# Optimization experiments

Measured on AMD Instinct MI355X. Metric: run time of the kernel, lower is better.

The kernel has to match this reference:

```python
import jax, jax.numpy as jnp
import numpy as np
import math

B, L = 4, 4096
D_MODEL = 1024
D_INNER = 1024          # expand=1
D_STATE = 1             # required by rearrange 'b d 1 l' in ssm()
D_CONV = 2
DT_RANK = 64            # ceil(1024/16)
EPS = 1e-5


def setup_inputs() -> dict:
    key = jax.random.key(0)
    ks = jax.random.split(key, 8)
    dt_min, dt_max, dt_floor = 1e-3, 1e-1, 1e-4
    # dt_proj bias init: inverse-softplus of log-uniform dt (faithful to dt_init)
    dt = jnp.exp(jax.random.uniform(ks[5], (D_INNER,)) * (math.log(dt_max) - math.log(dt_min)) + math.log(dt_min))
    dt = jnp.clip(dt, dt_floor, None)
    inv_dt = dt + jnp.log(-jnp.expm1(-dt))
    std = DT_RANK ** -0.5
    return {
        "x": jax.random.normal(ks[0], (B, L, D_MODEL), dtype=jnp.float32),
        "w_in": jax.random.normal(ks[1], (2 * D_INNER, D_MODEL), dtype=jnp.float32) * 0.02,
        "conv_w": jax.random.normal(ks[2], (D_INNER, 1, D_CONV), dtype=jnp.float32) * 0.5,
        "conv_b": jnp.zeros((D_INNER,), dtype=jnp.float32),
        "x_proj_weight": jax.random.normal(ks[3], (DT_RANK + 2 * D_STATE, D_INNER), dtype=jnp.float32) * 0.02,
        "dt_projs_weight": jax.random.uniform(ks[4], (D_INNER, DT_RANK), minval=-std, maxval=std, dtype=jnp.float32),
        "dt_projs_bias": inv_dt,
        "A_logs": jnp.tile(jnp.log(jnp.arange(1, D_STATE + 1, dtype=jnp.float32))[None, :], (D_INNER, 1)),
        "Ds": jnp.ones((D_INNER,), dtype=jnp.float32),
        "ln_w": jnp.ones((D_INNER,), dtype=jnp.float32),
        "ln_b": jnp.zeros((D_INNER,), dtype=jnp.float32),
        "w_out": jax.random.normal(ks[6], (D_MODEL, D_INNER), dtype=jnp.float32) * 0.02,
    }


def _selective_scan(u, delta, A, Bs):
    # u, delta: (B, D, L); A: (D, N); Bs: (B, N, L) -> hidden states h: (B, D, N, L)
    dA = jnp.exp(jnp.einsum('bdl,dn->bdnl', delta, A))            # (B,D,N,L)
    dBu = jnp.einsum('bdl,bnl,bdl->bdnl', delta, Bs, u)           # delta * B * u
    dA_t = jnp.moveaxis(dA, -1, 0)                                # (L,B,D,N)
    dBu_t = jnp.moveaxis(dBu, -1, 0)

    def step(h, inp):
        a_t, bu_t = inp
        h = a_t * h + bu_t
        return h, h

    h0 = jnp.zeros(dA.shape[:-1], dtype=u.dtype)
    _, hs = jax.lax.scan(step, h0, (dA_t, dBu_t))                 # (L,B,D,N)
    return jnp.moveaxis(hs, 0, -1)                                # (B,D,N,L)


def reference(x, w_in, conv_w, conv_b, x_proj_weight, dt_projs_weight,
              dt_projs_bias, A_logs, Ds, ln_w, ln_b, w_out):
    Bsz, Lsz, _ = x.shape
    # in_proj (bias=False), chunk into x and gate z
    xz = x @ w_in.T                                               # (B,L,2*D)
    xc, z = xz[..., :D_INNER], xz[..., D_INNER:]
    xc = jnp.transpose(xc, (0, 2, 1))                             # (B,D,L)
    # depthwise causal conv1d, padding=d_conv-1, truncated to L
    xc = jax.lax.conv_general_dilated(
        xc, conv_w, window_strides=(1,), padding=[(D_CONV - 1, D_CONV - 1)],
        feature_group_count=D_INNER,
        dimension_numbers=('NCH', 'OIH', 'NCH'))[..., :Lsz]
    xc = xc + conv_b[None, :, None]
    xc = jax.nn.silu(xc)
    # ssm()
    x_dbl = jnp.einsum('rd,bdl->brl', x_proj_weight, xc)          # (B,R+2N,L)
    dts = x_dbl[:, :DT_RANK]
    Bs = x_dbl[:, DT_RANK:DT_RANK + D_STATE]                      # (B,N,L)
    Cs = x_dbl[:, DT_RANK + D_STATE:]                             # (B,N,L)
    dts = jnp.einsum('dr,brl->bdl', dt_projs_weight, dts)         # (B,D,L)
    A = -jnp.exp(A_logs)                                          # (D,N)
    delta = jax.nn.softplus(dts + dt_projs_bias[None, :, None])   # delta_softplus=True
    h = _selective_scan(xc, delta, A, Bs)                         # (B,D,N,L)
    h = h.reshape(Bsz, D_INNER * D_STATE, Lsz)                    # 'b d 1 l -> b (d 1) l' (N==1)
    y = h * Cs + xc * Ds[:, None]                                 # (B,D,L)
    # out_norm (LayerNorm over d_inner), gate, out_proj
    y = jnp.transpose(y, (0, 2, 1))                               # (B,L,D)
    mu = jnp.mean(y, axis=-1, keepdims=True)
    var = jnp.mean(jnp.square(y - mu), axis=-1, keepdims=True)
    y = (y - mu) * jax.lax.rsqrt(var + EPS) * ln_w + ln_b
    y = y * jax.nn.silu(z)
    return y @ w_out.T                                            # (B,L,d_model)
```

## Files before the change

kernel.cpp:

```cpp
#include <hip/hip_runtime.h>
#include <hip/hip_bf16.h>
#include <cstdint>
#include <cstddef>

typedef short short8 __attribute__((ext_vector_type(8)));
typedef short short4v __attribute__((ext_vector_type(4)));
typedef float floatx4 __attribute__((ext_vector_type(4)));

constexpr int Bz = 4;
constexpr int Lz = 4096;
constexpr int Dm = 1024;
constexpr int Di = 1024;
constexpr int Mrows = Bz * Lz;
constexpr int CH  = 32;
constexpr int NCH = Lz / CH;
constexpr int XPJ_KS = 4;

__device__ __forceinline__ void load16(const void* g, void* l) {
  __builtin_amdgcn_global_load_lds((__attribute__((address_space(1))) void*)g,
                                   (__attribute__((address_space(3))) void*)l,
                                   16, 0, 0);
}

__device__ __forceinline__ float bf2f(const __hip_bfloat16 v) { return __bfloat162float(v); }
__device__ __forceinline__ short f2bfs(float v) {
  __hip_bfloat16 h = __float2bfloat16(v);
  return *(short*)&h;
}

__global__ __launch_bounds__(256) void cvt_all(
    const float* __restrict__ x, const float* __restrict__ w_in,
    const float* __restrict__ w_out, const float* __restrict__ xpw,
    const float* __restrict__ dtw,
    __hip_bfloat16* __restrict__ xbf, __hip_bfloat16* __restrict__ w_in_bf,
    __hip_bfloat16* __restrict__ w_out_bf, __hip_bfloat16* __restrict__ xpw_bf,
    __hip_bfloat16* __restrict__ dtw_bf)
{
  const int i = blockIdx.x * 256 + threadIdx.x;
  const float* src; __hip_bfloat16* dst; int j;
  if (i < 4194304)      { src = x;     dst = xbf;      j = i; }
  else if (i < 4718592) { src = w_in;  dst = w_in_bf;  j = i - 4194304; }
  else if (i < 4980736) { src = w_out; dst = w_out_bf; j = i - 4718592; }
  else if (i < 4997632) { src = xpw;   dst = xpw_bf;   j = i - 4980736; }
  else if (i < 5014016) { src = dtw;   dst = dtw_bf;   j = i - 4997632; }
  else return;
  const float4 v = ((const float4*)src)[j];
  short4v s;
  s[0] = f2bfs(v.x); s[1] = f2bfs(v.y); s[2] = f2bfs(v.z); s[3] = f2bfs(v.w);
  ((short4v*)dst)[j] = s;
}

template <int EPI>
__global__ __launch_bounds__(256) void gemm128(
    const __hip_bfloat16* __restrict__ A,
    const __hip_bfloat16* __restrict__ W,
    int K, int N,
    __hip_bfloat16* __restrict__ outb0,
    __hip_bfloat16* __restrict__ outb1,
    float* __restrict__ outf,
    const float* __restrict__ biasf)
{
  constexpr int BK = 32;
  constexpr int GY = 16;
  __shared__ short sA[128 * BK];
  __shared__ short sB[128 * BK];
  const int tid  = threadIdx.x;
  const int wid  = tid >> 6;
  const int lane = tid & 63;

  const int gx  = gridDim.x;
  const int id  = blockIdx.y * gx + blockIdx.x;
  const int seg = gx * GY;
  const int bx  = (id % seg) / GY;
  const int by  = (id / seg) * GY + (id % GY);

  const int m0 = by * 128;
  const int n0 = bx * 128;
  const int wm = (wid & 1) * 64;
  const int wn = (wid >> 1) * 64;

  floatx4 acc[4][4];
#pragma unroll
  for (int i = 0; i < 4; i++)
#pragma unroll
    for (int j = 0; j < 4; j++) acc[i][j] = (floatx4){0.f, 0.f, 0.f, 0.f};

  const short* Ag = (const short*)A + (size_t)(m0 + (tid >> 2)) * K + (tid & 3) * 8;
  const short* Bg = (const short*)W + (size_t)(n0 + (tid >> 2)) * K + (tid & 3) * 8;
  short* sAd = &sA[tid * 8];
  short* sBd = &sB[tid * 8];
  const size_t rstep = (size_t)64 * K;
  const int fr = lane & 15, fq = lane >> 4;

  for (int kb = 0; kb < K; kb += BK) {
    load16(Ag, sAd);
    load16(Ag + rstep, sAd + 2048);
    load16(Bg, sBd);
    load16(Bg + rstep, sBd + 2048);
    Ag += BK; Bg += BK;
    __syncthreads();

    short8 av[4], bv[4];
#pragma unroll
    for (int mt = 0; mt < 4; mt++) av[mt] = *(const short8*)&sA[(wm + mt * 16 + fr) * BK + fq * 8];
#pragma unroll
    for (int nt = 0; nt < 4; nt++) bv[nt] = *(const short8*)&sB[(wn + nt * 16 + fr) * BK + fq * 8];
#pragma unroll
    for (int mt = 0; mt < 4; mt++)
#pragma unroll
      for (int nt = 0; nt < 4; nt++)
        acc[mt][nt] = __builtin_amdgcn_mfma_f32_16x16x32_bf16(av[mt], bv[nt], acc[mt][nt], 0, 0, 0);
    __syncthreads();
  }

#pragma unroll
  for (int mt = 0; mt < 4; mt++) {
#pragma unroll
    for (int nt = 0; nt < 4; nt++) {
#pragma unroll
      for (int r = 0; r < 4; r++) {
        const int gm = m0 + wm + mt * 16 + fq * 4 + r;
        const int gn = n0 + wn + nt * 16 + fr;
        float v = acc[mt][nt][r];
        if constexpr (EPI == 0) {
          if (gn < 1024) outb0[(size_t)gm * 1024 + gn] = __float2bfloat16(v);
          else           outb1[(size_t)gm * 1024 + (gn - 1024)] = __float2bfloat16(v);
        } else if constexpr (EPI == 1) {
          v += biasf[gn];
          v = (v > 15.f) ? v : __logf(1.f + __expf(v));
          outb0[(size_t)gm * N + gn] = __float2bfloat16(v);
        } else {
          outf[(size_t)gm * N + gn] = v;
        }
      }
    }
  }
}

__device__ __forceinline__ void wait_lgkm0() {
  asm volatile("s_waitcnt lgkmcnt(0)");
  __builtin_amdgcn_sched_barrier(0);
}

template <int EPI>
__device__ __forceinline__ void cluster_mfma(int MQ, floatx4 (&acc)[8][4],
                                             const short8 (&av)[8][2],
                                             const short8 (&bv)[4][2])
{
  __builtin_amdgcn_s_setprio(1);
#pragma unroll
  for (int j = 0; j < 2; j++)
#pragma unroll
    for (int nf = 0; nf < 4; nf++)
#pragma unroll
      for (int ks = 0; ks < 2; ks++)
        acc[2 * MQ + j][nf] = __builtin_amdgcn_mfma_f32_16x16x32_bf16(
            av[2 * MQ + j][ks], bv[nf][ks], acc[2 * MQ + j][nf], 0, 0, 0);
  __builtin_amdgcn_s_setprio(0);
}

template <int EPI>
__global__ __launch_bounds__(512, 2) void gemm256(
    const __hip_bfloat16* __restrict__ A,
    const __hip_bfloat16* __restrict__ W,
    int K, int N,
    __hip_bfloat16* __restrict__ outb0,
    __hip_bfloat16* __restrict__ outb1,
    float* __restrict__ outf,
    const float* __restrict__ cw, const float* __restrict__ cb,
    __hip_bfloat16* __restrict__ xef, __hip_bfloat16* __restrict__ xel)
{
  __shared__ alignas(16) char lds[131072];
  const int tid  = threadIdx.x;
  const int wid  = tid >> 6;
  const int lane = tid & 63;
  const int wm = wid >> 2;
  const int wn = wid & 3;
  const int fr = lane & 15, fq = lane >> 4;

  const int gx   = gridDim.x;
  const int nwg  = gx * gridDim.y;
  const int orig = blockIdx.y * gx + blockIdx.x;
  const int swz  = (orig & 7) * (nwg >> 3) + (orig >> 3);
  const int bx   = swz % gx;
  const int by   = swz / gx;
  const int m0 = by * 256;
  const int n0 = bx * 256;
  const size_t K2 = (size_t)K * 2;

  int rowo[2], colo[2];
#pragma unroll
  for (int i = 0; i < 2; i++) {
    const int p = i * 8192 + tid * 16;
    const int s = p >> 10;
    const int r = (p >> 6) & 15;
    rowo[i] = (s >> 1) * 16 + r;
    colo[i] = (s & 1) * 64 + ((p & 63) ^ (((r >> 3) & 1) << 5));
  }
  const char* Ab = (const char*)A + (size_t)m0 * K2;
  const char* Bb = (const char*)W + (size_t)n0 * K2;
  char* lbase = (char*)lds;

#define STAGE_A(c, h, kt) do {                                                          \
    load16(Ab + (size_t)((h) * 128 + rowo[0]) * K2 + (size_t)(kt) * 128 + colo[0],      \
           lbase + (c) * 32768 + (h) * 16384 + tid * 16);                               \
    load16(Ab + (size_t)((h) * 128 + rowo[1]) * K2 + (size_t)(kt) * 128 + colo[1],      \
           lbase + (c) * 32768 + (h) * 16384 + 8192 + tid * 16);                        \
  } while (0)
#define STAGE_B(c, h, kt) do {                                                          \
    load16(Bb + (size_t)((h) * 128 + rowo[0]) * K2 + (size_t)(kt) * 128 + colo[0],      \
           lbase + 65536 + (c) * 32768 + (h) * 16384 + tid * 16);                       \
    load16(Bb + (size_t)((h) * 128 + rowo[1]) * K2 + (size_t)(kt) * 128 + colo[1],      \
           lbase + 65536 + (c) * 32768 + (h) * 16384 + 8192 + tid * 16);                \
  } while (0)

  const int foff = (fr * 64 + fq * 16) ^ (((fr >> 3) & 1) << 5);

  floatx4 acc[8][4];
#pragma unroll
  for (int i = 0; i < 8; i++)
#pragma unroll
    for (int j = 0; j < 4; j++) acc[i][j] = (floatx4){0.f, 0.f, 0.f, 0.f};

  STAGE_A(0, 0, 0); STAGE_A(0, 1, 0); STAGE_B(0, 0, 0); STAGE_B(0, 1, 0);
  STAGE_B(1, 0, 1); STAGE_B(1, 1, 1); STAGE_A(1, 0, 1);
  asm volatile("s_waitcnt vmcnt(6)");
  __builtin_amdgcn_sched_barrier(0);
  __builtin_amdgcn_s_barrier();

  const int NT = K >> 6;
  short8 av[8][2], bv[4][2];
#pragma unroll 2
  for (int t = 0; t < NT; ++t) {
    const int cur = t & 1, nxt = cur ^ 1;
    const char* la = lbase + cur * 32768 + wm * 16384 + foff;
    const char* lb = lbase + 65536 + cur * 32768 + (wn >> 1) * 16384 + (wn & 1) * 8192 + foff;

#pragma unroll
    for (int nf = 0; nf < 4; nf++)
#pragma unroll
      for (int ks = 0; ks < 2; ks++)
        bv[nf][ks] = *(const short8*)(lb + (nf * 2 + ks) * 1024);
#pragma unroll
    for (int mf = 0; mf < 2; mf++)
#pragma unroll
      for (int ks = 0; ks < 2; ks++)
        av[mf][ks] = *(const short8*)(la + (mf * 2 + ks) * 1024);
    if (t + 1 < NT) STAGE_A(nxt, 1, t + 1);
    wait_lgkm0();
    cluster_mfma<EPI>(0, acc, av, bv);
    __builtin_amdgcn_s_barrier();

#pragma unroll
    for (int mf = 2; mf < 4; mf++)
#pragma unroll
      for (int ks = 0; ks < 2; ks++)
        av[mf][ks] = *(const short8*)(la + (mf * 2 + ks) * 1024);
    if (t + 2 < NT) STAGE_B(cur, 0, t + 2);
    wait_lgkm0();
    cluster_mfma<EPI>(1, acc, av, bv);
    __builtin_amdgcn_s_barrier();

#pragma unroll
    for (int mf = 4; mf < 8; mf++)
#pragma unroll
      for (int ks = 0; ks < 2; ks++)
        av[mf][ks] = *(const short8*)(la + (mf * 2 + ks) * 1024);
    if (t + 2 < NT) STAGE_B(cur, 1, t + 2);
    wait_lgkm0();
    cluster_mfma<EPI>(2, acc, av, bv);
    __builtin_amdgcn_s_barrier();

    if (t + 2 < NT) STAGE_A(cur, 0, t + 2);
    cluster_mfma<EPI>(3, acc, av, bv);
    if (t < NT - 2) {
      asm volatile("s_waitcnt vmcnt(6)");
      __builtin_amdgcn_sched_barrier(0);
      __builtin_amdgcn_s_barrier();
    } else if (t == NT - 2) {
      asm volatile("s_waitcnt vmcnt(0)");
      __builtin_amdgcn_sched_barrier(0);
      __builtin_amdgcn_s_barrier();
    }
  }
#undef STAGE_A
#undef STAGE_B

  if constexpr (EPI == 0) {
    if (n0 < 1024) {
      short* lt = (short*)lds;
#pragma unroll
      for (int mf = 0; mf < 8; mf++)
#pragma unroll
        for (int nf = 0; nf < 4; nf++)
#pragma unroll
          for (int r = 0; r < 4; r++)
            lt[(wm * 128 + mf * 16 + fq * 4 + r) * 256 + wn * 64 + nf * 16 + fr] =
                f2bfs(acc[mf][nf][r]);
      __syncthreads();

      const int lrow0 = wid * 2 + (lane >> 5);
      const int c8 = (lane & 31) * 8;
      const int d0 = n0 + c8;
      const float4* cw4 = (const float4*)(cw + 2 * d0);
      const float4 wA = cw4[0], wB = cw4[1], wC = cw4[2], wD = cw4[3];
      const float w0a[8] = {wA.x, wA.z, wB.x, wB.z, wC.x, wC.z, wD.x, wD.z};
      const float w1a[8] = {wA.y, wA.w, wB.y, wB.w, wC.y, wC.w, wD.y, wD.w};
      const float4* cb4 = (const float4*)(cb + d0);
      const float4 b0 = cb4[0], b1 = cb4[1];
      const float ba[8] = {b0.x, b0.y, b0.z, b0.w, b1.x, b1.y, b1.z, b1.w};
      const int tix = m0 >> 8;

      for (int it = 0; it < 16; ++it) {
        const int rl = lrow0 + it * 16;
        const short8 curv = *(const short8*)&lt[rl * 256 + c8];
        if (rl == 0)   *(short8*)((short*)xef + tix * 1024 + d0) = curv;
        if (rl == 255) *(short8*)((short*)xel + tix * 1024 + d0) = curv;
        if (rl == 0) continue;
        const short8 prvv = *(const short8*)&lt[(rl - 1) * 256 + c8];
        short8 outv;
#pragma unroll
        for (int k = 0; k < 8; k++) {
          const float pc = __uint_as_float(((uint32_t)(uint16_t)prvv[k]) << 16);
          const float cc = __uint_as_float(((uint32_t)(uint16_t)curv[k]) << 16);
          const float v = pc * w0a[k] + cc * w1a[k] + ba[k];
          outv[k] = f2bfs(v / (1.f + __expf(-v)));
        }
        *(short8*)((short*)outb0 + (size_t)(m0 + rl) * 1024 + d0) = outv;
      }
    } else {
#pragma unroll
      for (int mf = 0; mf < 8; mf++)
#pragma unroll
        for (int nf = 0; nf < 4; nf++)
#pragma unroll
          for (int r = 0; r < 4; r++) {
            const int gm = m0 + wm * 128 + mf * 16 + fq * 4 + r;
            const int gn = n0 + wn * 64 + nf * 16 + fr;
            outb1[(size_t)gm * 1024 + (gn - 1024)] = __float2bfloat16(acc[mf][nf][r]);
          }
    }
  } else {
#pragma unroll
    for (int mf = 0; mf < 8; mf++)
#pragma unroll
      for (int nf = 0; nf < 4; nf++)
#pragma unroll
        for (int r = 0; r < 4; r++) {
          const int gm = m0 + wm * 128 + mf * 16 + fq * 4 + r;
          const int gn = n0 + wn * 64 + nf * 16 + fr;
          outf[(size_t)gm * N + gn] = acc[mf][nf][r];
        }
  }
}

__global__ __launch_bounds__(256) void conv_fix(
    const __hip_bfloat16* __restrict__ xef, const __hip_bfloat16* __restrict__ xel,
    const float* __restrict__ cw, const float* __restrict__ cb,
    __hip_bfloat16* __restrict__ u)
{
  const int i8 = (blockIdx.x * 256 + threadIdx.x) * 8;
  const int T  = i8 >> 10;
  const int d0 = i8 & 1023;
  const short8 cur = *(const short8*)((const short*)xef + T * 1024 + d0);
  short8 prv;
  if (T & 15) prv = *(const short8*)((const short*)xel + (T - 1) * 1024 + d0);
  else        prv = (short8){0, 0, 0, 0, 0, 0, 0, 0};
  const float4* cw4 = (const float4*)(cw + 2 * d0);
  const float4 wA = cw4[0], wB = cw4[1], wC = cw4[2], wD = cw4[3];
  const float w0a[8] = {wA.x, wA.z, wB.x, wB.z, wC.x, wC.z, wD.x, wD.z};
  const float w1a[8] = {wA.y, wA.w, wB.y, wB.w, wC.y, wC.w, wD.y, wD.w};
  const float4* cb4 = (const float4*)(cb + d0);
  const float4 b0 = cb4[0], b1 = cb4[1];
  const float ba[8] = {b0.x, b0.y, b0.z, b0.w, b1.x, b1.y, b1.z, b1.w};
  short8 outv;
#pragma unroll
  for (int k = 0; k < 8; k++) {
    const float pc = __uint_as_float(((uint32_t)(uint16_t)prv[k]) << 16);
    const float cc = __uint_as_float(((uint32_t)(uint16_t)cur[k]) << 16);
    const float v = pc * w0a[k] + cc * w1a[k] + ba[k];
    outv[k] = f2bfs(v / (1.f + __expf(-v)));
  }
  *(short8*)((short*)u + (size_t)T * 256 * 1024 + d0) = outv;
}

__global__ __launch_bounds__(256) void gemm_xproj(
    const __hip_bfloat16* __restrict__ A,
    const __hip_bfloat16* __restrict__ W,
    float* __restrict__ part)
{
  constexpr int K = 1024, BK = 32, KC = K / XPJ_KS;
  __shared__ short sA[128 * BK];
  __shared__ short sB[80 * BK];
  const int tid = threadIdx.x;
  const int wid = tid >> 6, lane = tid & 63;
  const int kc = blockIdx.x;
  const int m0 = blockIdx.y * 128;

  floatx4 acc[2][5];
#pragma unroll
  for (int i = 0; i < 2; i++)
#pragma unroll
    for (int j = 0; j < 5; j++) acc[i][j] = (floatx4){0.f, 0.f, 0.f, 0.f};

  const short* Ag = (const short*)A + (size_t)(m0 + (tid >> 2)) * K + kc * KC + (tid & 3) * 8;
  const int brow2 = 64 + (tid >> 2);
  const int brow2c = brow2 > 65 ? 65 : brow2;
  const short* Bg  = (const short*)W + (size_t)(tid >> 2) * K + kc * KC + (tid & 3) * 8;
  const short* Bg2 = (const short*)W + (size_t)brow2c * K + kc * KC + (tid & 3) * 8;
  const size_t rstep = (size_t)64 * K;
  const int fr = lane & 15, fq = lane >> 4;

  for (int kb = 0; kb < KC; kb += BK) {
    load16(Ag, &sA[tid * 8]);
    load16(Ag + rstep, &sA[2048 + tid * 8]);
    load16(Bg, &sB[tid * 8]);
    if (tid < 64) load16(Bg2, &sB[2048 + tid * 8]);
    Ag += BK; Bg += BK; Bg2 += BK;
    __syncthreads();

    short8 av[2], bv[5];
#pragma unroll
    for (int mt = 0; mt < 2; mt++) av[mt] = *(const short8*)&sA[(wid * 32 + mt * 16 + fr) * BK + fq * 8];
#pragma unroll
    for (int nt = 0; nt < 5; nt++) bv[nt] = *(const short8*)&sB[(nt * 16 + fr) * BK + fq * 8];
#pragma unroll
    for (int mt = 0; mt < 2; mt++)
#pragma unroll
      for (int nt = 0; nt < 5; nt++)
        acc[mt][nt] = __builtin_amdgcn_mfma_f32_16x16x32_bf16(av[mt], bv[nt], acc[mt][nt], 0, 0, 0);
    __syncthreads();
  }

  float* pp = part + (size_t)kc * Mrows * 66;
#pragma unroll
  for (int mt = 0; mt < 2; mt++) {
#pragma unroll
    for (int nt = 0; nt < 5; nt++) {
#pragma unroll
      for (int r = 0; r < 4; r++) {
        const int gm = m0 + wid * 32 + mt * 16 + fq * 4 + r;
        const int gn = nt * 16 + fr;
        if (gn < 66) pp[(size_t)gm * 66 + gn] = acc[mt][nt][r];
      }
    }
  }
}

__global__ __launch_bounds__(256) void xproj_reduce(
    const float* __restrict__ part,
    __hip_bfloat16* __restrict__ dts,
    float* __restrict__ Bs, float* __restrict__ Cs)
{
  const int i = blockIdx.x * 256 + threadIdx.x;
  if (i >= Mrows * 66) return;
  const int gm = i / 66, gn = i - gm * 66;
  float s = part[i] + part[i + (size_t)Mrows * 66]
          + part[i + (size_t)2 * Mrows * 66] + part[i + (size_t)3 * Mrows * 66];
  if (gn < 64)       dts[(size_t)gm * 64 + gn] = __float2bfloat16(s);
  else if (gn == 64) Bs[gm] = s;
  else               Cs[gm] = s;
}

__global__ __launch_bounds__(256) void scan_p1(
    const __hip_bfloat16* __restrict__ delta, const __hip_bfloat16* __restrict__ u,
    const float* __restrict__ Bsv, const float* __restrict__ A_logs,
    float* __restrict__ carryP, float* __restrict__ carryS)
{
  const int dp = blockIdx.x * 256 + threadIdx.x;
  const int d  = dp * 2;
  const int c = blockIdx.y, b = blockIdx.z;
  const float2 Al = *(const float2*)(A_logs + d);
  const float Ac0 = -__expf(Al.x), Ac1 = -__expf(Al.y);
  const size_t base = ((size_t)(b * Lz + c * CH)) * Di + d;
  const float* Bp = Bsv + (size_t)b * Lz + c * CH;
  float P0 = 1.f, h0 = 0.f, P1 = 1.f, h1 = 0.f;
#pragma unroll 8
  for (int j = 0; j < CH; j++) {
    const uint32_t dv = *(const uint32_t*)((const uint16_t*)delta + base + (size_t)j * Di);
    const uint32_t uv = *(const uint32_t*)((const uint16_t*)u + base + (size_t)j * Di);
    const float dl0 = __uint_as_float(dv << 16);
    const float dl1 = __uint_as_float(dv & 0xffff0000u);
    const float uu0 = __uint_as_float(uv << 16);
    const float uu1 = __uint_as_float(uv & 0xffff0000u);
    const float bj  = Bp[j];
    const float a0 = __expf(dl0 * Ac0), a1 = __expf(dl1 * Ac1);
    h0 = a0 * h0 + dl0 * bj * uu0;
    h1 = a1 * h1 + dl1 * bj * uu1;
    P0 *= a0; P1 *= a1;
  }
  const size_t ci = ((size_t)(b * NCH + c)) * Di + d;
  *(float2*)(carryP + ci) = make_float2(P0, P1);
  *(float2*)(carryS + ci) = make_float2(h0, h1);
}

__global__ __launch_bounds__(64) void scan_p2(
    const float* __restrict__ carryP, const float* __restrict__ carryS,
    float* __restrict__ hin)
{
  const int t = blockIdx.x * 64 + threadIdx.x;
  const int b = t >> 10, d = t & (Di - 1);
  float h = 0.f;
  for (int c = 0; c < NCH; c++) {
    const size_t ci = ((size_t)(b * NCH + c)) * Di + d;
    hin[ci] = h;
    h = carryP[ci] * h + carryS[ci];
  }
}

__global__ __launch_bounds__(256) void scan_p3(
    const __hip_bfloat16* __restrict__ delta, __hip_bfloat16* __restrict__ uy,
    const float* __restrict__ Bsv, const float* __restrict__ Csv,
    const float* __restrict__ A_logs, const float* __restrict__ Ds,
    const float* __restrict__ hin)
{
  const int dp = blockIdx.x * 256 + threadIdx.x;
  const int d  = dp * 2;
  const int c = blockIdx.y, b = blockIdx.z;
  const float2 Al = *(const float2*)(A_logs + d);
  const float Ac0 = -__expf(Al.x), Ac1 = -__expf(Al.y);
  const float2 Dd = *(const float2*)(Ds + d);
  const size_t base = ((size_t)(b * Lz + c * CH)) * Di + d;
  const float* Bp = Bsv + (size_t)b * Lz + c * CH;
  const float* Cp = Csv + (size_t)b * Lz + c * CH;
  const size_t ci = ((size_t)(b * NCH + c)) * Di + d;
  const float2 hh = *(const float2*)(hin + ci);
  float h0 = hh.x, h1 = hh.y;
#pragma unroll 8
  for (int j = 0; j < CH; j++) {
    const size_t ix = base + (size_t)j * Di;
    const uint32_t dv = *(const uint32_t*)((const uint16_t*)delta + ix);
    const uint32_t uv = *(const uint32_t*)((const uint16_t*)uy + ix);
    const float dl0 = __uint_as_float(dv << 16);
    const float dl1 = __uint_as_float(dv & 0xffff0000u);
    const float uu0 = __uint_as_float(uv << 16);
    const float uu1 = __uint_as_float(uv & 0xffff0000u);
    const float bj = Bp[j], cj = Cp[j];
    const float a0 = __expf(dl0 * Ac0), a1 = __expf(dl1 * Ac1);
    h0 = a0 * h0 + dl0 * bj * uu0;
    h1 = a1 * h1 + dl1 * bj * uu1;
    const float y0 = h0 * cj + uu0 * Dd.x;
    const float y1 = h1 * cj + uu1 * Dd.y;
    const uint32_t o = (uint32_t)(uint16_t)f2bfs(y0) | ((uint32_t)(uint16_t)f2bfs(y1) << 16);
    *(uint32_t*)((uint16_t*)uy + ix) = o;
  }
}

__global__ __launch_bounds__(256) void ln_gate(
    const __hip_bfloat16* __restrict__ y, const __hip_bfloat16* __restrict__ z,
    const float* __restrict__ lnw, const float* __restrict__ lnb,
    __hip_bfloat16* __restrict__ yg)
{
  const int row = blockIdx.x;
  const int tid = threadIdx.x;
  const int wid = tid >> 6, lane = tid & 63;
  const short4v yv = *(const short4v*)((const short*)y + (size_t)row * Di + tid * 4);
  const short4v zv4 = *(const short4v*)((const short*)z + (size_t)row * Di + tid * 4);
  float v[4];
#pragma unroll
  for (int i = 0; i < 4; i++)
    v[i] = __uint_as_float(((uint32_t)(uint16_t)yv[i]) << 16);
  float s1 = v[0] + v[1] + v[2] + v[3];
  float s2 = v[0] * v[0] + v[1] * v[1] + v[2] * v[2] + v[3] * v[3];
#pragma unroll
  for (int o = 32; o > 0; o >>= 1) {
    s1 += __shfl_down(s1, o, 64);
    s2 += __shfl_down(s2, o, 64);
  }
  __shared__ float r1[4], r2[4];
  if (lane == 0) { r1[wid] = s1; r2[wid] = s2; }
  __syncthreads();
  const float t1 = r1[0] + r1[1] + r1[2] + r1[3];
  const float t2 = r2[0] + r2[1] + r2[2] + r2[3];
  const float mu = t1 * (1.f / Di);
  const float var = t2 * (1.f / Di) - mu * mu;
  const float rstd = rsqrtf(var + 1e-5f);

  const float4 wv = ((const float4*)lnw)[tid];
  const float4 bv = ((const float4*)lnb)[tid];
  const float wa[4] = {wv.x, wv.y, wv.z, wv.w};
  const float ba[4] = {bv.x, bv.y, bv.z, bv.w};
  short4v og;
#pragma unroll
  for (int i = 0; i < 4; i++) {
    const float zz = __uint_as_float(((uint32_t)(uint16_t)zv4[i]) << 16);
    const float g = zz / (1.f + __expf(-zz));
    og[i] = f2bfs(((v[i] - mu) * rstd * wa[i] + ba[i]) * g);
  }
  *(short4v*)((short*)yg + (size_t)row * Di + tid * 4) = og;
}

__global__ __launch_bounds__(256) void fill_diag(float* __restrict__ out, int n, float val)
{
  const int i = blockIdx.x * 256 + threadIdx.x;
  if (i < n) out[i] = val;
}

extern "C" void kernel_launch(void* const* d_in, const int* in_sizes, int n_in,
                              void* d_out, int out_size, void* d_ws, size_t ws_size,
                              hipStream_t stream)
{
  const float* x      = (const float*)d_in[0];
  const float* w_in   = (const float*)d_in[1];
  const float* conv_w = (const float*)d_in[2];
  const float* conv_b = (const float*)d_in[3];
  const float* xpw    = (const float*)d_in[4];
  const float* dtw    = (const float*)d_in[5];
  const float* dtb    = (const float*)d_in[6];
  const float* A_logs = (const float*)d_in[7];
  const float* Ds     = (const float*)d_in[8];
  const float* lnw    = (const float*)d_in[9];
  const float* lnb    = (const float*)d_in[10];
  const float* w_out  = (const float*)d_in[11];
  float* outF = (float*)d_out;

  const size_t BF16BIG  = (size_t)Mrows * Di * sizeof(__hip_bfloat16);
  const size_t NEED_RUN = 69603328;

  if (ws_size < NEED_RUN) {
    fill_diag<<<(out_size + 255) / 256, 256, 0, stream>>>(
        outF, out_size, (float)(ws_size >> 10));
    return;
  }

  uint8_t* ws = (uint8_t*)d_ws;
  size_t off = 0;
  auto alloc = [&](size_t bytes) { void* p = ws + off; off += (bytes + 255) & ~(size_t)255; return p; };

  __hip_bfloat16* slotA    = (__hip_bfloat16*)alloc(BF16BIG);
  __hip_bfloat16* slotC    = (__hip_bfloat16*)alloc(BF16BIG);
  __hip_bfloat16* w_out_bf = (__hip_bfloat16*)alloc((size_t)Dm * Di * 2);
  __hip_bfloat16* xpw_bf   = (__hip_bfloat16*)alloc((size_t)66 * Di * 2);
  __hip_bfloat16* dtw_bf   = (__hip_bfloat16*)alloc((size_t)Di * 64 * 2);
  float* Bsv = (float*)alloc((size_t)Mrows * sizeof(float));
  float* Csv = (float*)alloc((size_t)Mrows * sizeof(float));

  __hip_bfloat16* zbuf    = (__hip_bfloat16*)d_out;
  __hip_bfloat16* w_in_bf = (__hip_bfloat16*)((uint8_t*)d_out + 33554432);
  __hip_bfloat16* dts     = (__hip_bfloat16*)((uint8_t*)d_out + 37748736);
  float* carryP = (float*)((uint8_t*)d_out + 39845888);
  float* carryS = (float*)((uint8_t*)d_out + 41943040);
  float* hin    = (float*)((uint8_t*)d_out + 44040192);
  __hip_bfloat16* xef = (__hip_bfloat16*)((uint8_t*)d_out + 46137344);
  __hip_bfloat16* xel = (__hip_bfloat16*)((uint8_t*)d_out + 46137344 + 131072);
  float* xpj_part = (float*)((uint8_t*)d_out + 41943040);

  __hip_bfloat16* xbf   = slotC;
  __hip_bfloat16* ubuf  = slotA;
  __hip_bfloat16* delta = slotC;
  __hip_bfloat16* yg    = slotC;

  cvt_all<<<(5014016 + 255) / 256, 256, 0, stream>>>(
      x, w_in, w_out, xpw, dtw, xbf, w_in_bf, w_out_bf, xpw_bf, dtw_bf);

  gemm256<0><<<dim3(2 * Di / 256, Mrows / 256), 512, 0, stream>>>(
      xbf, w_in_bf, Dm, 2 * Di, ubuf, zbuf, nullptr, conv_w, conv_b, xef, xel);
  conv_fix<<<32, 256, 0, stream>>>(xef, xel, conv_w, conv_b, ubuf);
  gemm_xproj<<<dim3(XPJ_KS, Mrows / 128), 256, 0, stream>>>(ubuf, xpw_bf, xpj_part);
  xproj_reduce<<<(Mrows * 66 + 255) / 256, 256, 0, stream>>>(xpj_part, dts, Bsv, Csv);
  gemm128<1><<<dim3(Di / 128, Mrows / 128), 256, 0, stream>>>(
      dts, dtw_bf, 64, Di, delta, nullptr, nullptr, dtb);
  scan_p1<<<dim3(Di / 512, NCH, Bz), 256, 0, stream>>>(delta, ubuf, Bsv, A_logs, carryP, carryS);
  scan_p2<<<(Bz * Di) / 64, 64, 0, stream>>>(carryP, carryS, hin);
  scan_p3<<<dim3(Di / 512, NCH, Bz), 256, 0, stream>>>(delta, ubuf, Bsv, Csv, A_logs, Ds, hin);
  ln_gate<<<Mrows, 256, 0, stream>>>(ubuf, zbuf, lnw, lnb, yg);
  gemm256<1><<<dim3(Dm / 256, Mrows / 256), 512, 0, stream>>>(
      yg, w_out_bf, Di, Dm, nullptr, nullptr, outF, nullptr, nullptr, nullptr, nullptr);
}
```

Baseline: 351.2 us.

## Fuse scan output with LayerNorm gate and swizzle GEMM epilogue LDS tile

The final scan phase now handles one full row of 1024 channels per 512-thread block. It applies LayerNorm, SiLU gating and the bf16 store inline, which removes the separate ln_gate kernel and the write-back and re-read of the scan output. Each timestep now needs a cross-wave reduction and a __syncthreads, the grid shrinks to one block per chunk and batch, and loop unrolling is dropped, so the scan may become latency-bound. Separately, the in-projection GEMM's LDS staging tile for the conv epilogue gets an XOR column swizzle to reduce bank conflicts.

```diff
diff --git a/kernel.cpp b/kernel.cpp
--- a/kernel.cpp
+++ b/kernel.cpp
@@ -142,6 +142,10 @@
   __builtin_amdgcn_sched_barrier(0);
 }
 
+__device__ __forceinline__ int ltix(int row, int col) {
+  return row * 256 + (col ^ (((row >> 2) & 3) << 4));
+}
+
 template <int EPI>
 __device__ __forceinline__ void cluster_mfma(int MQ, floatx4 (&acc)[8][4],
                                              const short8 (&av)[8][2],
@@ -294,9 +298,11 @@
 #pragma unroll
         for (int nf = 0; nf < 4; nf++)
 #pragma unroll
-          for (int r = 0; r < 4; r++)
-            lt[(wm * 128 + mf * 16 + fq * 4 + r) * 256 + wn * 64 + nf * 16 + fr] =
-                f2bfs(acc[mf][nf][r]);
+          for (int r = 0; r < 4; r++) {
+            const int srow = wm * 128 + mf * 16 + fq * 4 + r;
+            const int scol = wn * 64 + nf * 16 + fr;
+            lt[ltix(srow, scol)] = f2bfs(acc[mf][nf][r]);
+          }
       __syncthreads();
 
       const int lrow0 = wid * 2 + (lane >> 5);
@@ -313,11 +319,11 @@
 
       for (int it = 0; it < 16; ++it) {
         const int rl = lrow0 + it * 16;
-        const short8 curv = *(const short8*)&lt[rl * 256 + c8];
+        const short8 curv = *(const short8*)&lt[ltix(rl, c8)];
         if (rl == 0)   *(short8*)((short*)xef + tix * 1024 + d0) = curv;
         if (rl == 255) *(short8*)((short*)xel + tix * 1024 + d0) = curv;
         if (rl == 0) continue;
-        const short8 prvv = *(const short8*)&lt[(rl - 1) * 256 + c8];
+        const short8 prvv = *(const short8*)&lt[ltix(rl - 1, c8)];
         short8 outv;
 #pragma unroll
         for (int k = 0; k < 8; k++) {
@@ -508,29 +514,35 @@
   }
 }
 
-__global__ __launch_bounds__(256) void scan_p3(
-    const __hip_bfloat16* __restrict__ delta, __hip_bfloat16* __restrict__ uy,
+__global__ __launch_bounds__(512) void scan_p3_ln(
+    const __hip_bfloat16* __restrict__ delta, const __hip_bfloat16* __restrict__ u,
     const float* __restrict__ Bsv, const float* __restrict__ Csv,
     const float* __restrict__ A_logs, const float* __restrict__ Ds,
-    const float* __restrict__ hin)
-{
-  const int dp = blockIdx.x * 256 + threadIdx.x;
+    const float* __restrict__ hin, const __hip_bfloat16* __restrict__ z,
+    const float* __restrict__ lnw, const float* __restrict__ lnb,
+    __hip_bfloat16* __restrict__ yg)
+{
+  const int dp = threadIdx.x;
   const int d  = dp * 2;
-  const int c = blockIdx.y, b = blockIdx.z;
+  const int c = blockIdx.x, b = blockIdx.y;
+  const int wid = dp >> 6, lane = dp & 63;
   const float2 Al = *(const float2*)(A_logs + d);
   const float Ac0 = -__expf(Al.x), Ac1 = -__expf(Al.y);
   const float2 Dd = *(const float2*)(Ds + d);
+  const float2 wv = *(const float2*)(lnw + d);
+  const float2 bw = *(const float2*)(lnb + d);
   const size_t base = ((size_t)(b * Lz + c * CH)) * Di + d;
   const float* Bp = Bsv + (size_t)b * Lz + c * CH;
   const float* Cp = Csv + (size_t)b * Lz + c * CH;
   const size_t ci = ((size_t)(b * NCH + c)) * Di + d;
   const float2 hh = *(const float2*)(hin + ci);
   float h0 = hh.x, h1 = hh.y;
-#pragma unroll 8
+  __shared__ float r1[2][8], r2[2][8];
+
   for (int j = 0; j < CH; j++) {
     const size_t ix = base + (size_t)j * Di;
     const uint32_t dv = *(const uint32_t*)((const uint16_t*)delta + ix);
-    const uint32_t uv = *(const uint32_t*)((const uint16_t*)uy + ix);
+    const uint32_t uv = *(const uint32_t*)((const uint16_t*)u + ix);
     const float dl0 = __uint_as_float(dv << 16);
     const float dl1 = __uint_as_float(dv & 0xffff0000u);
     const float uu0 = __uint_as_float(uv << 16);
@@ -541,53 +553,33 @@
     h1 = a1 * h1 + dl1 * bj * uu1;
     const float y0 = h0 * cj + uu0 * Dd.x;
     const float y1 = h1 * cj + uu1 * Dd.y;
-    const uint32_t o = (uint32_t)(uint16_t)f2bfs(y0) | ((uint32_t)(uint16_t)f2bfs(y1) << 16);
-    *(uint32_t*)((uint16_t*)uy + ix) = o;
-  }
-}
-
-__global__ __launch_bounds__(256) void ln_gate(
-    const __hip_bfloat16* __restrict__ y, const __hip_bfloat16* __restrict__ z,
-    const float* __restrict__ lnw, const float* __restrict__ lnb,
-    __hip_bfloat16* __restrict__ yg)
-{
-  const int row = blockIdx.x;
-  const int tid = threadIdx.x;
-  const int wid = tid >> 6, lane = tid & 63;
-  const short4v yv = *(const short4v*)((const short*)y + (size_t)row * Di + tid * 4);
-  const short4v zv4 = *(const short4v*)((const short*)z + (size_t)row * Di + tid * 4);
-  float v[4];
-#pragma unroll
-  for (int i = 0; i < 4; i++)
-    v[i] = __uint_as_float(((uint32_t)(uint16_t)yv[i]) << 16);
-  float s1 = v[0] + v[1] + v[2] + v[3];
-  float s2 = v[0] * v[0] + v[1] * v[1] + v[2] * v[2] + v[3] * v[3];
-#pragma unroll
-  for (int o = 32; o > 0; o >>= 1) {
-    s1 += __shfl_down(s1, o, 64);
-    s2 += __shfl_down(s2, o, 64);
-  }
-  __shared__ float r1[4], r2[4];
-  if (lane == 0) { r1[wid] = s1; r2[wid] = s2; }
-  __syncthreads();
-  const float t1 = r1[0] + r1[1] + r1[2] + r1[3];
-  const float t2 = r2[0] + r2[1] + r2[2] + r2[3];
-  const float mu = t1 * (1.f / Di);
-  const float var = t2 * (1.f / Di) - mu * mu;
-  const float rstd = rsqrtf(var + 1e-5f);
-
-  const float4 wv = ((const float4*)lnw)[tid];
-  const float4 bv = ((const float4*)lnb)[tid];
-  const float wa[4] = {wv.x, wv.y, wv.z, wv.w};
-  const float ba[4] = {bv.x, bv.y, bv.z, bv.w};
-  short4v og;
-#pragma unroll
-  for (int i = 0; i < 4; i++) {
-    const float zz = __uint_as_float(((uint32_t)(uint16_t)zv4[i]) << 16);
-    const float g = zz / (1.f + __expf(-zz));
-    og[i] = f2bfs(((v[i] - mu) * rstd * wa[i] + ba[i]) * g);
-  }
-  *(short4v*)((short*)yg + (size_t)row * Di + tid * 4) = og;
+
+    float s1 = y0 + y1;
+    float s2 = y0 * y0 + y1 * y1;
+#pragma unroll
+    for (int o = 32; o > 0; o >>= 1) {
+      s1 += __shfl_down(s1, o, 64);
+      s2 += __shfl_down(s2, o, 64);
+    }
+    if (lane == 0) { r1[j & 1][wid] = s1; r2[j & 1][wid] = s2; }
+    __syncthreads();
+    float t1 = 0.f, t2 = 0.f;
+#pragma unroll
+    for (int w = 0; w < 8; w++) { t1 += r1[j & 1][w]; t2 += r2[j & 1][w]; }
+    const float mu = t1 * (1.f / Di);
+    const float var = t2 * (1.f / Di) - mu * mu;
+    const float rstd = rsqrtf(var + 1e-5f);
+
+    const uint32_t zv = *(const uint32_t*)((const uint16_t*)z + ix);
+    const float z0 = __uint_as_float(zv << 16);
+    const float z1 = __uint_as_float(zv & 0xffff0000u);
+    const float g0 = z0 / (1.f + __expf(-z0));
+    const float g1 = z1 / (1.f + __expf(-z1));
+    const float o0 = ((y0 - mu) * rstd * wv.x + bw.x) * g0;
+    const float o1 = ((y1 - mu) * rstd * wv.y + bw.y) * g1;
+    const uint32_t ov = (uint32_t)(uint16_t)f2bfs(o0) | ((uint32_t)(uint16_t)f2bfs(o1) << 16);
+    *(uint32_t*)((uint16_t*)yg + ix) = ov;
+  }
 }
 
 __global__ __launch_bounds__(256) void fill_diag(float* __restrict__ out, int n, float val)
@@ -662,8 +654,8 @@
       dts, dtw_bf, 64, Di, delta, nullptr, nullptr, dtb);
   scan_p1<<<dim3(Di / 512, NCH, Bz), 256, 0, stream>>>(delta, ubuf, Bsv, A_logs, carryP, carryS);
   scan_p2<<<(Bz * Di) / 64, 64, 0, stream>>>(carryP, carryS, hin);
-  scan_p3<<<dim3(Di / 512, NCH, Bz), 256, 0, stream>>>(delta, ubuf, Bsv, Csv, A_logs, Ds, hin);
-  ln_gate<<<Mrows, 256, 0, stream>>>(ubuf, zbuf, lnw, lnb, yg);
+  scan_p3_ln<<<dim3(NCH, Bz), 512, 0, stream>>>(
+      delta, ubuf, Bsv, Csv, A_logs, Ds, hin, zbuf, lnw, lnb, yg);
   gemm256<1><<<dim3(Dm / 256, Mrows / 256), 512, 0, stream>>>(
       yg, w_out_bf, Di, Dm, nullptr, nullptr, outF, nullptr, nullptr, nullptr, nullptr);
 }
```

After: 354.4 us. No clear change (+0.9%).
